# Performance work log

Measured on AMD Instinct MI355X. Metric: run time of the kernel, lower is better.

Reference implementation:

```python
import jax, jax.numpy as jnp
import numpy as np

WH, WW = 8, 8
DIM, HEADS = 512, 16
HEAD_DIM = DIM // HEADS
SCALE = HEAD_DIM ** (-0.5)
N = WH * WW
NW = 64  # number of windows sharing one mask


def _relative_position_index(wh, ww):
    ch, cw = np.meshgrid(np.arange(wh), np.arange(ww), indexing='ij')
    coords = np.stack([ch, cw]).reshape(2, -1)              # (2, N)
    rel = coords[:, :, None] - coords[:, None, :]           # (2, N, N)
    rel = rel.transpose(1, 2, 0).astype(np.int64)           # (N, N, 2)
    rel[:, :, 0] += wh - 1
    rel[:, :, 1] += ww - 1
    rel[:, :, 0] *= 2 * ww - 1
    return jnp.asarray(rel.sum(-1))                         # (N, N) int

_REL_IDX = _relative_position_index(WH, WW)


def setup_inputs() -> dict:
    key = jax.random.key(0)
    ks = jax.random.split(key, 10)
    B_ = 4096
    q = jax.random.normal(ks[0], (B_, N, DIM), dtype=jnp.float32)
    kv = jax.random.normal(ks[1], (B_, N, DIM), dtype=jnp.float32)
    mask = jax.random.normal(ks[2], (NW, N, N), dtype=jnp.float32)
    Wq = jax.random.normal(ks[3], (DIM, DIM), dtype=jnp.float32) * (DIM ** -0.5)
    bq = jnp.zeros((DIM,), dtype=jnp.float32)
    Wkv = jax.random.normal(ks[4], (DIM, 2 * DIM), dtype=jnp.float32) * (DIM ** -0.5)
    bkv = jnp.zeros((2 * DIM,), dtype=jnp.float32)
    bias_table = jax.random.normal(ks[5], ((2 * WH - 1) * (2 * WW - 1), HEADS), dtype=jnp.float32) * 0.02
    Wp = jax.random.normal(ks[6], (DIM, DIM), dtype=jnp.float32) * (DIM ** -0.5)
    bp = jnp.zeros((DIM,), dtype=jnp.float32)
    return {'q': q, 'kv': kv, 'mask': mask, 'Wq': Wq, 'bq': bq,
            'Wkv': Wkv, 'bkv': bkv, 'bias_table': bias_table, 'Wp': Wp, 'bp': bp}


def reference(q, kv, mask, Wq, bq, Wkv, bkv, bias_table, Wp, bp):
    B_, N_q, C = q.shape
    N_kv = kv.shape[1]
    # projections
    qh = (q @ Wq + bq).reshape(B_, N_q, HEADS, HEAD_DIM).transpose(0, 2, 1, 3)  # bhqd
    kvh = (kv @ Wkv + bkv).reshape(B_, N_kv, 2, HEADS, HEAD_DIM)
    k = kvh[:, :, 0].transpose(0, 2, 1, 3)   # bhkd
    v = kvh[:, :, 1].transpose(0, 2, 1, 3)   # bhkd
    attn = jnp.einsum('bhqd,bhkd->bhqk', qh * SCALE, k)
    # relative position bias: (N, N, H) -> (H, N, N)
    rpb = bias_table[_REL_IDX].transpose(2, 0, 1)
    attn = attn + rpb[None]
    # additive window mask
    nW = mask.shape[0]
    attn = attn.reshape(B_ // nW, nW, HEADS, N_q, N_kv) + mask[None, :, None]
    attn = attn.reshape(B_, HEADS, N_q, N_kv)
    attn = jax.nn.softmax(attn, axis=-1)
    x = jnp.einsum('bhqk,bhkd->bhqd', attn, v).transpose(0, 2, 1, 3).reshape(B_, N_q, C)
    return x @ Wp + bp
```

## Files before the change

### kernel.cpp

```cpp
#include <hip/hip_runtime.h>

typedef short bf16x8 __attribute__((ext_vector_type(8)));
typedef unsigned short u16x8 __attribute__((ext_vector_type(8)));
typedef float f32x4 __attribute__((ext_vector_type(4)));

#define MFMA16(a, b, c) __builtin_amdgcn_mfma_f32_16x16x32_bf16((a), (b), (c), 0, 0, 0)

#define SCALEF 0.17677669529663687f

__device__ __forceinline__ unsigned short f2bf(float f) {
  union { float f; unsigned u; } v; v.f = f;
  unsigned r = v.u + 0x7fffu + ((v.u >> 16) & 1u);
  return (unsigned short)(r >> 16);
}

__device__ __forceinline__ void gl_lds16(const void* g, void* l) {
  __builtin_amdgcn_global_load_lds(
      (const __attribute__((address_space(1))) void*)g,
      (__attribute__((address_space(3))) void*)l, 16, 0, 0);
}

__global__ __launch_bounds__(256) void transpose_cvt_k(const float* __restrict__ W,
    unsigned short* __restrict__ Wt, int K, int N) {
  int i = blockIdx.x * 256 + threadIdx.x;
  if (i >= N * K) return;
  int n = i / K, k = i - n * K;
  Wt[i] = f2bf(W[(long)k * N + n]);
}

__global__ __launch_bounds__(256) void build_rpb_k(const float* __restrict__ bt,
    float* __restrict__ rpb) {
  int i = blockIdx.x * 256 + threadIdx.x;
  if (i >= 16 * 64 * 64) return;
  int h = i >> 12, q = (i >> 6) & 63, k = i & 63;
  int dh = (q >> 3) - (k >> 3) + 7;
  int dw = (q & 7) - (k & 7) + 7;
  rpb[i] = bt[(dh * 15 + dw) * 16 + h];
}

__global__ __launch_bounds__(256) void cvt_bf16_k(const float* __restrict__ in,
    unsigned short* __restrict__ out, int n8) {
  int i = blockIdx.x * 256 + threadIdx.x;
  if (i >= n8) return;
  const float4* p = (const float4*)(in + (size_t)i * 8);
  float4 a = p[0], b = p[1];
  uint4 pk;
  pk.x = (unsigned)f2bf(a.x) | ((unsigned)f2bf(a.y) << 16);
  pk.y = (unsigned)f2bf(a.z) | ((unsigned)f2bf(a.w) << 16);
  pk.z = (unsigned)f2bf(b.x) | ((unsigned)f2bf(b.y) << 16);
  pk.w = (unsigned)f2bf(b.z) | ((unsigned)f2bf(b.w) << 16);
  *(uint4*)(out + (size_t)i * 8) = pk;
}

template <typename OT>
__device__ __forceinline__ void gemm_body(const unsigned short* __restrict__ A,
    const unsigned short* __restrict__ Bt, const float* __restrict__ bias,
    OT* __restrict__ C, int M, int N, int K)
{
  constexpr bool O_F32 = (sizeof(OT) == 4);

  __shared__ __align__(16) char smem[32768];
  unsigned short* Asm = (unsigned short*)smem;
  unsigned short* Bsm = Asm + 8192;

  const int tn = N >> 7;
  const int nbm = M >> 7;
  const int g = blockIdx.x;
  const int xcd = g & 7;
  const int s = g >> 3;
  const int bm = xcd * (nbm >> 3) + (s / tn);
  const int bn = s - (s / tn) * tn;

  const int tid = threadIdx.x;
  const int wave = tid >> 6, lane = tid & 63;
  const int wr = wave >> 1, wc = wave & 1;
  const int lg = lane >> 4, lc = lane & 15;

  const long rowBase = (long)bm * 128;
  const int colBase = bn * 128;
  const int KT = K >> 6;

  f32x4 acc[4][4];
#pragma unroll
  for (int i = 0; i < 4; ++i)
#pragma unroll
    for (int j = 0; j < 4; ++j)
      acc[i][j] = f32x4{0.f, 0.f, 0.f, 0.f};

  const int blr = lane >> 3;
  const int bsw = (lane & 7) ^ blr;

  auto issueA = [&](int kt) {
#pragma unroll
    for (int j = 0; j < 4; ++j) {
      int r = j * 32 + wave * 8 + blr;
      gl_lds16(A + (rowBase + r) * (long)K + kt * 64 + bsw * 8,
               Asm + (j * 4 + wave) * 512);
    }
  };
  auto issueB = [&](int kt) {
#pragma unroll
    for (int j = 0; j < 4; ++j) {
      int r = j * 32 + wave * 8 + blr;
      gl_lds16(Bt + (long)(colBase + r) * K + kt * 64 + bsw * 8,
               Bsm + (j * 4 + wave) * 512);
    }
  };
  auto compute = [&]() {
#pragma unroll
    for (int ks = 0; ks < 2; ++ks) {
      const int ca = (ks * 4 + lg) ^ (lc & 7);
      bf16x8 af[4], bfr[4];
#pragma unroll
      for (int mt = 0; mt < 4; ++mt)
        af[mt] = *(const bf16x8*)(Asm + (wr * 64 + mt * 16 + lc) * 64 + ca * 8);
#pragma unroll
      for (int nt = 0; nt < 4; ++nt)
        bfr[nt] = *(const bf16x8*)(Bsm + (wc * 64 + nt * 16 + lc) * 64 + ca * 8);
#pragma unroll
      for (int mt = 0; mt < 4; ++mt)
#pragma unroll
        for (int nt = 0; nt < 4; ++nt)
          acc[mt][nt] = MFMA16(af[mt], bfr[nt], acc[mt][nt]);
    }
  };

  issueA(0); issueB(0);
  __syncthreads();

  for (int kt = 0; kt < KT; ++kt) {
    const bool more = (kt + 1 < KT);
    compute();
    __syncthreads();
    if (more) {
      issueA(kt + 1); issueB(kt + 1);
      __syncthreads();
    }
  }

  float bv[4];
#pragma unroll
  for (int nt = 0; nt < 4; ++nt)
    bv[nt] = bias[colBase + wc * 64 + nt * 16 + lc];

  if constexpr (O_F32) {
    float* Sf = (float*)smem;
#pragma unroll
    for (int h = 0; h < 2; ++h) {
      if (wr == h) {
#pragma unroll
        for (int mt = 0; mt < 4; ++mt)
#pragma unroll
          for (int nt = 0; nt < 4; ++nt)
#pragma unroll
            for (int r = 0; r < 4; ++r)
              Sf[(mt * 16 + lg * 4 + r) * 128 + wc * 64 + nt * 16 + lc] =
                  acc[mt][nt][r] + bv[nt];
      }
      __syncthreads();
#pragma unroll
      for (int p = 0; p < 8; ++p) {
        int ch = p * 256 + tid, row = ch >> 5, c = ch & 31;
        *(float4*)((float*)C + (rowBase + h * 64 + row) * N + colBase + c * 4) =
            *(const float4*)(Sf + row * 128 + c * 4);
      }
      __syncthreads();
    }
  } else {
    unsigned short* Su = (unsigned short*)smem;
#pragma unroll
    for (int h = 0; h < 2; ++h) {
      if (wr == h) {
#pragma unroll
        for (int mt = 0; mt < 4; ++mt)
#pragma unroll
          for (int nt = 0; nt < 4; ++nt)
#pragma unroll
            for (int r = 0; r < 4; ++r)
              Su[(mt * 16 + lg * 4 + r) * 128 + wc * 64 + nt * 16 + lc] =
                  f2bf(acc[mt][nt][r] + bv[nt]);
      }
      __syncthreads();
#pragma unroll
      for (int p = 0; p < 4; ++p) {
        int ch = p * 256 + tid, row = ch >> 4, c = ch & 15;
        *(uint4*)((unsigned short*)C + (rowBase + h * 64 + row) * N + colBase + c * 8) =
            *(const uint4*)(Su + row * 128 + c * 8);
      }
      __syncthreads();
    }
  }
}

__global__ __launch_bounds__(256, 4) void gemm_q_k(const unsigned short* __restrict__ A,
    const unsigned short* __restrict__ Bt, const float* __restrict__ bias,
    unsigned short* __restrict__ C, int M, int N, int K) {
  gemm_body<unsigned short>(A, Bt, bias, C, M, N, K);
}
__global__ __launch_bounds__(256, 4) void gemm_kv_k(const unsigned short* __restrict__ A,
    const unsigned short* __restrict__ Bt, const float* __restrict__ bias,
    unsigned short* __restrict__ C, int M, int N, int K) {
  gemm_body<unsigned short>(A, Bt, bias, C, M, N, K);
}
__global__ __launch_bounds__(256, 4) void gemm_out_k(const unsigned short* __restrict__ A,
    const unsigned short* __restrict__ Bt, const float* __restrict__ bias,
    float* __restrict__ C, int M, int N, int K) {
  gemm_body<float>(A, Bt, bias, C, M, N, K);
}

__global__ __launch_bounds__(256) void attn_k(
    const unsigned short* __restrict__ qh,
    const unsigned short* __restrict__ kvh,
    const float* __restrict__ mask,
    const float* __restrict__ rpb,
    unsigned short* __restrict__ x)
{
  __shared__ unsigned short P[4][64][72];
  __shared__ unsigned short Vt[4][32][72];

  const int b = blockIdx.x;
  const int w = b & 63;
  const int tid = threadIdx.x;
  const int wave = tid >> 6, lane = tid & 63;
  const int lg = lane >> 4, lc = lane & 15;
  const long rowQ = (long)b * 64;

  for (int hi = 0; hi < 4; ++hi) {
    const int h = wave * 4 + hi;

    bf16x8 qf[4], kf[4];
#pragma unroll
    for (int mt = 0; mt < 4; ++mt)
      qf[mt] = *(const bf16x8*)(qh + (rowQ + mt * 16 + lc) * 512 + h * 32 + lg * 8);
#pragma unroll
    for (int nt = 0; nt < 4; ++nt)
      kf[nt] = *(const bf16x8*)(kvh + (rowQ + nt * 16 + lc) * 1024 + h * 32 + lg * 8);

    f32x4 acc[4][4];
#pragma unroll
    for (int mt = 0; mt < 4; ++mt)
#pragma unroll
      for (int nt = 0; nt < 4; ++nt)
        acc[mt][nt] = f32x4{0.f, 0.f, 0.f, 0.f};
#pragma unroll
    for (int mt = 0; mt < 4; ++mt)
#pragma unroll
      for (int nt = 0; nt < 4; ++nt)
        acc[mt][nt] = MFMA16(qf[mt], kf[nt], acc[mt][nt]);

    {
      const unsigned short* vp = kvh + (rowQ + lane) * 1024 + 512 + h * 32;
      u16x8 v0 = *(const u16x8*)(vp);
      u16x8 v1 = *(const u16x8*)(vp + 8);
      u16x8 v2 = *(const u16x8*)(vp + 16);
      u16x8 v3 = *(const u16x8*)(vp + 24);
#pragma unroll
      for (int j = 0; j < 8; ++j) {
        Vt[wave][j][lane]      = v0[j];
        Vt[wave][8 + j][lane]  = v1[j];
        Vt[wave][16 + j][lane] = v2[j];
        Vt[wave][24 + j][lane] = v3[j];
      }
    }

    float pden[4][4];
#pragma unroll
    for (int mt = 0; mt < 4; ++mt) {
#pragma unroll
      for (int r = 0; r < 4; ++r) {
        const int qrow = mt * 16 + lg * 4 + r;
        const float* rp = rpb + h * 4096 + qrow * 64 + lc;
        const float* mp = mask + w * 4096 + qrow * 64 + lc;
        float sc[4];
#pragma unroll
        for (int nt = 0; nt < 4; ++nt)
          sc[nt] = acc[mt][nt][r] * SCALEF + rp[nt * 16] + mp[nt * 16];
        float mx = fmaxf(fmaxf(sc[0], sc[1]), fmaxf(sc[2], sc[3]));
        mx = fmaxf(mx, __shfl_xor(mx, 1));
        mx = fmaxf(mx, __shfl_xor(mx, 2));
        mx = fmaxf(mx, __shfl_xor(mx, 4));
        mx = fmaxf(mx, __shfl_xor(mx, 8));
        float s = 0.f;
#pragma unroll
        for (int nt = 0; nt < 4; ++nt) { sc[nt] = __expf(sc[nt] - mx); s += sc[nt]; }
        s += __shfl_xor(s, 1);
        s += __shfl_xor(s, 2);
        s += __shfl_xor(s, 4);
        s += __shfl_xor(s, 8);
        pden[mt][r] = 1.f / s;
#pragma unroll
        for (int nt = 0; nt < 4; ++nt)
          P[wave][qrow][nt * 16 + lc] = f2bf(sc[nt]);
      }
    }

    f32x4 xacc[4][2];
#pragma unroll
    for (int mt = 0; mt < 4; ++mt)
#pragma unroll
      for (int nt = 0; nt < 2; ++nt)
        xacc[mt][nt] = f32x4{0.f, 0.f, 0.f, 0.f};
#pragma unroll
    for (int ks = 0; ks < 2; ++ks) {
      bf16x8 pa[4], vb[2];
#pragma unroll
      for (int mt = 0; mt < 4; ++mt)
        pa[mt] = *(const bf16x8*)&P[wave][mt * 16 + lc][ks * 32 + lg * 8];
#pragma unroll
      for (int nt = 0; nt < 2; ++nt)
        vb[nt] = *(const bf16x8*)&Vt[wave][nt * 16 + lc][ks * 32 + lg * 8];
#pragma unroll
      for (int mt = 0; mt < 4; ++mt)
#pragma unroll
        for (int nt = 0; nt < 2; ++nt)
          xacc[mt][nt] = MFMA16(pa[mt], vb[nt], xacc[mt][nt]);
    }

#pragma unroll
    for (int mt = 0; mt < 4; ++mt)
#pragma unroll
      for (int nt = 0; nt < 2; ++nt)
#pragma unroll
        for (int r = 0; r < 4; ++r) {
          const int qrow = mt * 16 + lg * 4 + r;
          x[(rowQ + qrow) * 512 + h * 32 + nt * 16 + lc] =
              f2bf(xacc[mt][nt][r] * pden[mt][r]);
        }
  }
}

extern "C" void kernel_launch(void* const* d_in, const int* in_sizes, int n_in,
                              void* d_out, int out_size, void* d_ws, size_t ws_size,
                              hipStream_t stream) {
  const float* q    = (const float*)d_in[0];
  const float* kv   = (const float*)d_in[1];
  const float* mask = (const float*)d_in[2];
  const float* Wq   = (const float*)d_in[3];
  const float* bq   = (const float*)d_in[4];
  const float* Wkv  = (const float*)d_in[5];
  const float* bkv  = (const float*)d_in[6];
  const float* btab = (const float*)d_in[7];
  const float* Wp   = (const float*)d_in[8];
  const float* bp   = (const float*)d_in[9];
  float* out = (float*)d_out;

  const int M = 4096 * 64;

  char* ws = (char*)d_ws;
  const size_t OFF_QH   = 0;
  const size_t OFF_KVH  = OFF_QH + (size_t)M * 512 * 2;
  const size_t OFF_SCR  = OFF_KVH + (size_t)M * 1024 * 2;
  const size_t OFF_WQT  = OFF_SCR + (size_t)M * 512 * 2;
  const size_t OFF_WKVT = OFF_WQT + 512 * 512 * 2;
  const size_t OFF_WPT  = OFF_WKVT + 1024 * 512 * 2;
  const size_t OFF_RPB  = OFF_WPT + 512 * 512 * 2;

  unsigned short* qh    = (unsigned short*)(ws + OFF_QH);
  unsigned short* kvh   = (unsigned short*)(ws + OFF_KVH);
  unsigned short* scr   = (unsigned short*)(ws + OFF_SCR);
  unsigned short* Wq_t  = (unsigned short*)(ws + OFF_WQT);
  unsigned short* Wkv_t = (unsigned short*)(ws + OFF_WKVT);
  unsigned short* Wp_t  = (unsigned short*)(ws + OFF_WPT);
  float* rpbf           = (float*)(ws + OFF_RPB);

  transpose_cvt_k<<<(512 * 512 + 255) / 256, 256, 0, stream>>>(Wq, Wq_t, 512, 512);
  transpose_cvt_k<<<(512 * 1024 + 255) / 256, 256, 0, stream>>>(Wkv, Wkv_t, 512, 1024);
  transpose_cvt_k<<<(512 * 512 + 255) / 256, 256, 0, stream>>>(Wp, Wp_t, 512, 512);
  build_rpb_k<<<(16 * 64 * 64 + 255) / 256, 256, 0, stream>>>(btab, rpbf);

  const int n8 = M * 512 / 8;

  cvt_bf16_k<<<n8 / 256, 256, 0, stream>>>(kv, scr, n8);
  gemm_kv_k<<<(M / 128) * (1024 / 128), 256, 0, stream>>>(scr, Wkv_t, bkv, kvh, M, 1024, 512);

  cvt_bf16_k<<<n8 / 256, 256, 0, stream>>>(q, scr, n8);
  gemm_q_k<<<(M / 128) * (512 / 128), 256, 0, stream>>>(scr, Wq_t, bq, qh, M, 512, 512);

  attn_k<<<4096, 256, 0, stream>>>(qh, kvh, mask, rpbf, scr);

  gemm_out_k<<<(M / 128) * (512 / 128), 256, 0, stream>>>(scr, Wp_t, bp, out, M, 512, 512);

  (void)in_sizes; (void)n_in; (void)out_size; (void)ws_size;
}
```

Measured before the change: 1.577 ms.

## Precombine bias+mask into swizzled table and prefetch next-head Q/K in attention

```diff
diff --git a/kernel.cpp b/kernel.cpp
--- a/kernel.cpp
+++ b/kernel.cpp
@@ -28,14 +28,15 @@
   Wt[i] = f2bf(W[(long)k * N + n]);
 }
 
-__global__ __launch_bounds__(256) void build_rpb_k(const float* __restrict__ bt,
-    float* __restrict__ rpb) {
+__global__ __launch_bounds__(256) void build_cb2_k(const float* __restrict__ bt,
+    const float* __restrict__ mask, float* __restrict__ cb2) {
   int i = blockIdx.x * 256 + threadIdx.x;
-  if (i >= 16 * 64 * 64) return;
-  int h = i >> 12, q = (i >> 6) & 63, k = i & 63;
+  if (i >= 64 * 16 * 64 * 64) return;
+  int nt = i & 3, lc = (i >> 2) & 15, q = (i >> 6) & 63, h = (i >> 12) & 15, w = i >> 16;
+  int k = nt * 16 + lc;
   int dh = (q >> 3) - (k >> 3) + 7;
   int dw = (q & 7) - (k & 7) + 7;
-  rpb[i] = bt[(dh * 15 + dw) * 16 + h];
+  cb2[i] = bt[(dh * 15 + dw) * 16 + h] + mask[w * 4096 + q * 64 + k];
 }
 
 __global__ __launch_bounds__(256) void cvt_bf16_k(const float* __restrict__ in,
@@ -208,15 +209,15 @@
   gemm_body<float>(A, Bt, bias, C, M, N, K);
 }
 
-__global__ __launch_bounds__(256) void attn_k(
+__global__ __launch_bounds__(256, 3) void attn_k(
     const unsigned short* __restrict__ qh,
     const unsigned short* __restrict__ kvh,
-    const float* __restrict__ mask,
-    const float* __restrict__ rpb,
+    const float* __restrict__ cb2,
     unsigned short* __restrict__ x)
 {
-  __shared__ unsigned short P[4][64][72];
-  __shared__ unsigned short Vt[4][32][72];
+  constexpr int LP = 68;
+  __shared__ unsigned short P[4][64][LP];
+  __shared__ unsigned short Vt[4][32][LP];
 
   const int b = blockIdx.x;
   const int w = b & 63;
@@ -225,16 +226,32 @@
   const int lg = lane >> 4, lc = lane & 15;
   const long rowQ = (long)b * 64;
 
+  bf16x8 qf[2][4], kf[2][4];
+  u16x8 vr[4];
+
+  auto loadQK = [&](int h, int s2) {
+#pragma unroll
+    for (int mt = 0; mt < 4; ++mt)
+      qf[s2][mt] = *(const bf16x8*)(qh + (rowQ + mt * 16 + lc) * 512 + h * 32 + lg * 8);
+#pragma unroll
+    for (int nt = 0; nt < 4; ++nt)
+      kf[s2][nt] = *(const bf16x8*)(kvh + (rowQ + nt * 16 + lc) * 1024 + h * 32 + lg * 8);
+  };
+
+  loadQK(wave * 4, 0);
+
+#pragma unroll
   for (int hi = 0; hi < 4; ++hi) {
+    const int cur = hi & 1;
     const int h = wave * 4 + hi;
 
-    bf16x8 qf[4], kf[4];
-#pragma unroll
-    for (int mt = 0; mt < 4; ++mt)
-      qf[mt] = *(const bf16x8*)(qh + (rowQ + mt * 16 + lc) * 512 + h * 32 + lg * 8);
-#pragma unroll
-    for (int nt = 0; nt < 4; ++nt)
-      kf[nt] = *(const bf16x8*)(kvh + (rowQ + nt * 16 + lc) * 1024 + h * 32 + lg * 8);
+    {
+      const unsigned short* vp = kvh + (rowQ + lane) * 1024 + 512 + h * 32;
+      vr[0] = *(const u16x8*)(vp);
+      vr[1] = *(const u16x8*)(vp + 8);
+      vr[2] = *(const u16x8*)(vp + 16);
+      vr[3] = *(const u16x8*)(vp + 24);
+    }
 
     f32x4 acc[4][4];
 #pragma unroll
@@ -246,35 +263,22 @@
     for (int mt = 0; mt < 4; ++mt)
 #pragma unroll
       for (int nt = 0; nt < 4; ++nt)
-        acc[mt][nt] = MFMA16(qf[mt], kf[nt], acc[mt][nt]);
-
-    {
-      const unsigned short* vp = kvh + (rowQ + lane) * 1024 + 512 + h * 32;
-      u16x8 v0 = *(const u16x8*)(vp);
-      u16x8 v1 = *(const u16x8*)(vp + 8);
-      u16x8 v2 = *(const u16x8*)(vp + 16);
-      u16x8 v3 = *(const u16x8*)(vp + 24);
-#pragma unroll
-      for (int j = 0; j < 8; ++j) {
-        Vt[wave][j][lane]      = v0[j];
-        Vt[wave][8 + j][lane]  = v1[j];
-        Vt[wave][16 + j][lane] = v2[j];
-        Vt[wave][24 + j][lane] = v3[j];
-      }
-    }
-
+        acc[mt][nt] = MFMA16(qf[cur][mt], kf[cur][nt], acc[mt][nt]);
+
+    if (hi < 3) loadQK(h + 1, cur ^ 1);
+
+    const float* cbq = cb2 + (((size_t)(w * 16 + h)) << 12) + lc * 4;
     float pden[4][4];
 #pragma unroll
     for (int mt = 0; mt < 4; ++mt) {
 #pragma unroll
       for (int r = 0; r < 4; ++r) {
         const int qrow = mt * 16 + lg * 4 + r;
-        const float* rp = rpb + h * 4096 + qrow * 64 + lc;
-        const float* mp = mask + w * 4096 + qrow * 64 + lc;
+        f32x4 cb = *(const f32x4*)(cbq + qrow * 64);
         float sc[4];
 #pragma unroll
         for (int nt = 0; nt < 4; ++nt)
-          sc[nt] = acc[mt][nt][r] * SCALEF + rp[nt * 16] + mp[nt * 16];
+          sc[nt] = acc[mt][nt][r] * SCALEF + cb[nt];
         float mx = fmaxf(fmaxf(sc[0], sc[1]), fmaxf(sc[2], sc[3]));
         mx = fmaxf(mx, __shfl_xor(mx, 1));
         mx = fmaxf(mx, __shfl_xor(mx, 2));
@@ -292,6 +296,14 @@
         for (int nt = 0; nt < 4; ++nt)
           P[wave][qrow][nt * 16 + lc] = f2bf(sc[nt]);
       }
+    }
+
+#pragma unroll
+    for (int j = 0; j < 8; ++j) {
+      Vt[wave][j][lane]      = vr[0][j];
+      Vt[wave][8 + j][lane]  = vr[1][j];
+      Vt[wave][16 + j][lane] = vr[2][j];
+      Vt[wave][24 + j][lane] = vr[3][j];
     }
 
     f32x4 xacc[4][2];
@@ -353,7 +365,7 @@
   const size_t OFF_WQT  = OFF_SCR + (size_t)M * 512 * 2;
   const size_t OFF_WKVT = OFF_WQT + 512 * 512 * 2;
   const size_t OFF_WPT  = OFF_WKVT + 1024 * 512 * 2;
-  const size_t OFF_RPB  = OFF_WPT + 512 * 512 * 2;
+  const size_t OFF_CB2  = OFF_WPT + 512 * 512 * 2;
 
   unsigned short* qh    = (unsigned short*)(ws + OFF_QH);
   unsigned short* kvh   = (unsigned short*)(ws + OFF_KVH);
@@ -361,12 +373,12 @@
   unsigned short* Wq_t  = (unsigned short*)(ws + OFF_WQT);
   unsigned short* Wkv_t = (unsigned short*)(ws + OFF_WKVT);
   unsigned short* Wp_t  = (unsigned short*)(ws + OFF_WPT);
-  float* rpbf           = (float*)(ws + OFF_RPB);
+  float* cb2f           = (float*)(ws + OFF_CB2);
 
   transpose_cvt_k<<<(512 * 512 + 255) / 256, 256, 0, stream>>>(Wq, Wq_t, 512, 512);
   transpose_cvt_k<<<(512 * 1024 + 255) / 256, 256, 0, stream>>>(Wkv, Wkv_t, 512, 1024);
   transpose_cvt_k<<<(512 * 512 + 255) / 256, 256, 0, stream>>>(Wp, Wp_t, 512, 512);
-  build_rpb_k<<<(16 * 64 * 64 + 255) / 256, 256, 0, stream>>>(btab, rpbf);
+  build_cb2_k<<<(64 * 16 * 64 * 64) / 256, 256, 0, stream>>>(btab, mask, cb2f);
 
   const int n8 = M * 512 / 8;
 
@@ -376,7 +388,7 @@
   cvt_bf16_k<<<n8 / 256, 256, 0, stream>>>(q, scr, n8);
   gemm_q_k<<<(M / 128) * (512 / 128), 256, 0, stream>>>(scr, Wq_t, bq, qh, M, 512, 512);
 
-  attn_k<<<4096, 256, 0, stream>>>(qh, kvh, mask, rpbf, scr);
+  attn_k<<<4096, 256, 0, stream>>>(qh, kvh, cb2f, scr);
 
   gemm_out_k<<<(M / 128) * (512 / 128), 256, 0, stream>>>(scr, Wp_t, bp, out, M, 512, 512);
 
```

New measurement: 1.622 ms. 2.8% more time.

## Restructure attention kernel: per-wave query rows, shared V/mask in LDS, scale folded into Wq

Applied to the files above, without the earlier changes.

```diff
diff --git a/kernel.cpp b/kernel.cpp
--- a/kernel.cpp
+++ b/kernel.cpp
@@ -13,6 +13,10 @@
   unsigned r = v.u + 0x7fffu + ((v.u >> 16) & 1u);
   return (unsigned short)(r >> 16);
 }
+__device__ __forceinline__ float bf2f(unsigned short b) {
+  union { unsigned u; float f; } v; v.u = ((unsigned)b) << 16;
+  return v.f;
+}
 
 __device__ __forceinline__ void gl_lds16(const void* g, void* l) {
   __builtin_amdgcn_global_load_lds(
@@ -21,21 +25,28 @@
 }
 
 __global__ __launch_bounds__(256) void transpose_cvt_k(const float* __restrict__ W,
-    unsigned short* __restrict__ Wt, int K, int N) {
+    unsigned short* __restrict__ Wt, int K, int N, float scale) {
   int i = blockIdx.x * 256 + threadIdx.x;
   if (i >= N * K) return;
   int n = i / K, k = i - n * K;
-  Wt[i] = f2bf(W[(long)k * N + n]);
-}
-
-__global__ __launch_bounds__(256) void build_rpb_k(const float* __restrict__ bt,
-    float* __restrict__ rpb) {
+  Wt[i] = f2bf(W[(long)k * N + n] * scale);
+}
+
+__global__ __launch_bounds__(256) void scale_bias_k(const float* __restrict__ b,
+    float* __restrict__ bs, float scale, int n) {
+  int i = blockIdx.x * 256 + threadIdx.x;
+  if (i < n) bs[i] = b[i] * scale;
+}
+
+__global__ __launch_bounds__(256) void build_rpbp_k(const float* __restrict__ bt,
+    float* __restrict__ rpbp) {
   int i = blockIdx.x * 256 + threadIdx.x;
   if (i >= 16 * 64 * 64) return;
-  int h = i >> 12, q = (i >> 6) & 63, k = i & 63;
+  int kt = i & 3, lcv = (i >> 2) & 15, q = (i >> 6) & 63, h = i >> 12;
+  int k = kt * 16 + lcv;
   int dh = (q >> 3) - (k >> 3) + 7;
   int dw = (q & 7) - (k & 7) + 7;
-  rpb[i] = bt[(dh * 15 + dw) * 16 + h];
+  rpbp[i] = bt[(dh * 15 + dw) * 16 + h];
 }
 
 __global__ __launch_bounds__(256) void cvt_bf16_k(const float* __restrict__ in,
@@ -208,15 +219,17 @@
   gemm_body<float>(A, Bt, bias, C, M, N, K);
 }
 
-__global__ __launch_bounds__(256) void attn_k(
+__global__ __launch_bounds__(256, 5) void attn_k(
     const unsigned short* __restrict__ qh,
     const unsigned short* __restrict__ kvh,
     const float* __restrict__ mask,
-    const float* __restrict__ rpb,
+    const float* __restrict__ rpbp,
     unsigned short* __restrict__ x)
 {
-  __shared__ unsigned short P[4][64][72];
-  __shared__ unsigned short Vt[4][32][72];
+  __shared__ unsigned short P[64][68];
+  __shared__ unsigned short Vt[2][32][68];
+  __shared__ unsigned short maskS[64][68];
+  __shared__ unsigned short xs[4][16][40];
 
   const int b = blockIdx.x;
   const int w = b & 63;
@@ -225,107 +238,99 @@
   const int lg = lane >> 4, lc = lane & 15;
   const long rowQ = (long)b * 64;
 
-  for (int hi = 0; hi < 4; ++hi) {
-    const int h = wave * 4 + hi;
-
-    bf16x8 qf[4], kf[4];
-#pragma unroll
-    for (int mt = 0; mt < 4; ++mt)
-      qf[mt] = *(const bf16x8*)(qh + (rowQ + mt * 16 + lc) * 512 + h * 32 + lg * 8);
-#pragma unroll
-    for (int nt = 0; nt < 4; ++nt)
-      kf[nt] = *(const bf16x8*)(kvh + (rowQ + nt * 16 + lc) * 1024 + h * 32 + lg * 8);
-
-    f32x4 acc[4][4];
-#pragma unroll
-    for (int mt = 0; mt < 4; ++mt)
-#pragma unroll
-      for (int nt = 0; nt < 4; ++nt)
-        acc[mt][nt] = f32x4{0.f, 0.f, 0.f, 0.f};
-#pragma unroll
-    for (int mt = 0; mt < 4; ++mt)
-#pragma unroll
-      for (int nt = 0; nt < 4; ++nt)
-        acc[mt][nt] = MFMA16(qf[mt], kf[nt], acc[mt][nt]);
-
+#pragma unroll
+  for (int t = 0; t < 16; ++t) {
+    int i = t * 256 + tid;
+    int qq = i >> 6, k = i & 63;
+    maskS[qq][(k & 15) * 4 + (k >> 4)] = f2bf(mask[w * 4096 + i]);
+  }
+
+  const int vtok = tid >> 2, vg = tid & 3;
+  const unsigned short* vbase = kvh + (rowQ + vtok) * 1024 + 512 + vg * 8;
+
+  {
+    u16x8 v0 = *(const u16x8*)(vbase);
+#pragma unroll
+    for (int j = 0; j < 8; ++j) Vt[0][vg * 8 + j][vtok] = v0[j];
+  }
+  __syncthreads();
+
+  for (int h = 0; h < 16; ++h) {
+    const int cur = h & 1;
+
+    u16x8 vn;
+    if (h < 15) vn = *(const u16x8*)(vbase + (h + 1) * 32);
+
+    bf16x8 qf = *(const bf16x8*)(qh + (rowQ + wave * 16 + lc) * 512 + h * 32 + lg * 8);
+    bf16x8 kf[4];
+#pragma unroll
+    for (int kt = 0; kt < 4; ++kt)
+      kf[kt] = *(const bf16x8*)(kvh + (rowQ + kt * 16 + lc) * 1024 + h * 32 + lg * 8);
+
+    f32x4 acc[4];
+#pragma unroll
+    for (int kt = 0; kt < 4; ++kt) acc[kt] = f32x4{0.f, 0.f, 0.f, 0.f};
+#pragma unroll
+    for (int kt = 0; kt < 4; ++kt) acc[kt] = MFMA16(qf, kf[kt], acc[kt]);
+
+    float pden[4];
+#pragma unroll
+    for (int r = 0; r < 4; ++r) {
+      const int qrow = wave * 16 + lg * 4 + r;
+      f32x4 rp = *(const f32x4*)(rpbp + (h << 12) + qrow * 64 + lc * 4);
+      ushort4 mv = *(const ushort4*)&maskS[qrow][lc * 4];
+      float sc[4];
+      sc[0] = acc[0][r] + rp[0] + bf2f(mv.x);
+      sc[1] = acc[1][r] + rp[1] + bf2f(mv.y);
+      sc[2] = acc[2][r] + rp[2] + bf2f(mv.z);
+      sc[3] = acc[3][r] + rp[3] + bf2f(mv.w);
+      float mx = fmaxf(fmaxf(sc[0], sc[1]), fmaxf(sc[2], sc[3]));
+      mx = fmaxf(mx, __shfl_xor(mx, 1));
+      mx = fmaxf(mx, __shfl_xor(mx, 2));
+      mx = fmaxf(mx, __shfl_xor(mx, 4));
+      mx = fmaxf(mx, __shfl_xor(mx, 8));
+      float s = 0.f;
+#pragma unroll
+      for (int kt = 0; kt < 4; ++kt) { sc[kt] = __expf(sc[kt] - mx); s += sc[kt]; }
+      s += __shfl_xor(s, 1);
+      s += __shfl_xor(s, 2);
+      s += __shfl_xor(s, 4);
+      s += __shfl_xor(s, 8);
+      pden[r] = 1.f / s;
+#pragma unroll
+      for (int kt = 0; kt < 4; ++kt)
+        P[qrow][kt * 16 + lc] = f2bf(sc[kt]);
+    }
+
+    if (h < 15) {
+#pragma unroll
+      for (int j = 0; j < 8; ++j) Vt[cur ^ 1][vg * 8 + j][vtok] = vn[j];
+    }
+
+    f32x4 xacc[2];
+    xacc[0] = f32x4{0.f, 0.f, 0.f, 0.f};
+    xacc[1] = f32x4{0.f, 0.f, 0.f, 0.f};
+#pragma unroll
+    for (int ks = 0; ks < 2; ++ks) {
+      bf16x8 pa = *(const bf16x8*)&P[wave * 16 + lc][ks * 32 + lg * 8];
+      bf16x8 vb0 = *(const bf16x8*)&Vt[cur][lc][ks * 32 + lg * 8];
+      bf16x8 vb1 = *(const bf16x8*)&Vt[cur][16 + lc][ks * 32 + lg * 8];
+      xacc[0] = MFMA16(pa, vb0, xacc[0]);
+      xacc[1] = MFMA16(pa, vb1, xacc[1]);
+    }
+
+#pragma unroll
+    for (int dt = 0; dt < 2; ++dt)
+#pragma unroll
+      for (int r = 0; r < 4; ++r)
+        xs[wave][lg * 4 + r][dt * 16 + lc] = f2bf(xacc[dt][r] * pden[r]);
     {
-      const unsigned short* vp = kvh + (rowQ + lane) * 1024 + 512 + h * 32;
-      u16x8 v0 = *(const u16x8*)(vp);
-      u16x8 v1 = *(const u16x8*)(vp + 8);
-      u16x8 v2 = *(const u16x8*)(vp + 16);
-      u16x8 v3 = *(const u16x8*)(vp + 24);
-#pragma unroll
-      for (int j = 0; j < 8; ++j) {
-        Vt[wave][j][lane]      = v0[j];
-        Vt[wave][8 + j][lane]  = v1[j];
-        Vt[wave][16 + j][lane] = v2[j];
-        Vt[wave][24 + j][lane] = v3[j];
-      }
-    }
-
-    float pden[4][4];
-#pragma unroll
-    for (int mt = 0; mt < 4; ++mt) {
-#pragma unroll
-      for (int r = 0; r < 4; ++r) {
-        const int qrow = mt * 16 + lg * 4 + r;
-        const float* rp = rpb + h * 4096 + qrow * 64 + lc;
-        const float* mp = mask + w * 4096 + qrow * 64 + lc;
-        float sc[4];
-#pragma unroll
-        for (int nt = 0; nt < 4; ++nt)
-          sc[nt] = acc[mt][nt][r] * SCALEF + rp[nt * 16] + mp[nt * 16];
-        float mx = fmaxf(fmaxf(sc[0], sc[1]), fmaxf(sc[2], sc[3]));
-        mx = fmaxf(mx, __shfl_xor(mx, 1));
-        mx = fmaxf(mx, __shfl_xor(mx, 2));
-        mx = fmaxf(mx, __shfl_xor(mx, 4));
-        mx = fmaxf(mx, __shfl_xor(mx, 8));
-        float s = 0.f;
-#pragma unroll
-        for (int nt = 0; nt < 4; ++nt) { sc[nt] = __expf(sc[nt] - mx); s += sc[nt]; }
-        s += __shfl_xor(s, 1);
-        s += __shfl_xor(s, 2);
-        s += __shfl_xor(s, 4);
-        s += __shfl_xor(s, 8);
-        pden[mt][r] = 1.f / s;
-#pragma unroll
-        for (int nt = 0; nt < 4; ++nt)
-          P[wave][qrow][nt * 16 + lc] = f2bf(sc[nt]);
-      }
-    }
-
-    f32x4 xacc[4][2];
-#pragma unroll
-    for (int mt = 0; mt < 4; ++mt)
-#pragma unroll
-      for (int nt = 0; nt < 2; ++nt)
-        xacc[mt][nt] = f32x4{0.f, 0.f, 0.f, 0.f};
-#pragma unroll
-    for (int ks = 0; ks < 2; ++ks) {
-      bf16x8 pa[4], vb[2];
-#pragma unroll
-      for (int mt = 0; mt < 4; ++mt)
-        pa[mt] = *(const bf16x8*)&P[wave][mt * 16 + lc][ks * 32 + lg * 8];
-#pragma unroll
-      for (int nt = 0; nt < 2; ++nt)
-        vb[nt] = *(const bf16x8*)&Vt[wave][nt * 16 + lc][ks * 32 + lg * 8];
-#pragma unroll
-      for (int mt = 0; mt < 4; ++mt)
-#pragma unroll
-        for (int nt = 0; nt < 2; ++nt)
-          xacc[mt][nt] = MFMA16(pa[mt], vb[nt], xacc[mt][nt]);
-    }
-
-#pragma unroll
-    for (int mt = 0; mt < 4; ++mt)
-#pragma unroll
-      for (int nt = 0; nt < 2; ++nt)
-#pragma unroll
-        for (int r = 0; r < 4; ++r) {
-          const int qrow = mt * 16 + lg * 4 + r;
-          x[(rowQ + qrow) * 512 + h * 32 + nt * 16 + lc] =
-              f2bf(xacc[mt][nt][r] * pden[mt][r]);
-        }
+      int row = lane >> 2, c = lane & 3;
+      uint4 v = *(const uint4*)&xs[wave][row][c * 8];
+      *(uint4*)(x + (rowQ + wave * 16 + row) * 512 + h * 32 + c * 8) = v;
+    }
+
+    __syncthreads();
   }
 }
 
@@ -353,7 +358,8 @@
   const size_t OFF_WQT  = OFF_SCR + (size_t)M * 512 * 2;
   const size_t OFF_WKVT = OFF_WQT + 512 * 512 * 2;
   const size_t OFF_WPT  = OFF_WKVT + 1024 * 512 * 2;
-  const size_t OFF_RPB  = OFF_WPT + 512 * 512 * 2;
+  const size_t OFF_RPBP = OFF_WPT + 512 * 512 * 2;
+  const size_t OFF_BQS  = OFF_RPBP + 16 * 64 * 64 * 4;
 
   unsigned short* qh    = (unsigned short*)(ws + OFF_QH);
   unsigned short* kvh   = (unsigned short*)(ws + OFF_KVH);
@@ -361,12 +367,14 @@
   unsigned short* Wq_t  = (unsigned short*)(ws + OFF_WQT);
   unsigned short* Wkv_t = (unsigned short*)(ws + OFF_WKVT);
   unsigned short* Wp_t  = (unsigned short*)(ws + OFF_WPT);
-  float* rpbf           = (float*)(ws + OFF_RPB);
-
-  transpose_cvt_k<<<(512 * 512 + 255) / 256, 256, 0, stream>>>(Wq, Wq_t, 512, 512);
-  transpose_cvt_k<<<(512 * 1024 + 255) / 256, 256, 0, stream>>>(Wkv, Wkv_t, 512, 1024);
-  transpose_cvt_k<<<(512 * 512 + 255) / 256, 256, 0, stream>>>(Wp, Wp_t, 512, 512);
-  build_rpb_k<<<(16 * 64 * 64 + 255) / 256, 256, 0, stream>>>(btab, rpbf);
+  float* rpbp           = (float*)(ws + OFF_RPBP);
+  float* bq_s           = (float*)(ws + OFF_BQS);
+
+  transpose_cvt_k<<<(512 * 512 + 255) / 256, 256, 0, stream>>>(Wq, Wq_t, 512, 512, SCALEF);
+  transpose_cvt_k<<<(512 * 1024 + 255) / 256, 256, 0, stream>>>(Wkv, Wkv_t, 512, 1024, 1.0f);
+  transpose_cvt_k<<<(512 * 512 + 255) / 256, 256, 0, stream>>>(Wp, Wp_t, 512, 512, 1.0f);
+  scale_bias_k<<<2, 256, 0, stream>>>(bq, bq_s, SCALEF, 512);
+  build_rpbp_k<<<(16 * 64 * 64) / 256, 256, 0, stream>>>(btab, rpbp);
 
   const int n8 = M * 512 / 8;
 
@@ -374,9 +382,9 @@
   gemm_kv_k<<<(M / 128) * (1024 / 128), 256, 0, stream>>>(scr, Wkv_t, bkv, kvh, M, 1024, 512);
 
   cvt_bf16_k<<<n8 / 256, 256, 0, stream>>>(q, scr, n8);
-  gemm_q_k<<<(M / 128) * (512 / 128), 256, 0, stream>>>(scr, Wq_t, bq, qh, M, 512, 512);
-
-  attn_k<<<4096, 256, 0, stream>>>(qh, kvh, mask, rpbf, scr);
+  gemm_q_k<<<(M / 128) * (512 / 128), 256, 0, stream>>>(scr, Wq_t, bq_s, qh, M, 512, 512);
+
+  attn_k<<<4096, 256, 0, stream>>>(qh, kvh, mask, rpbp, scr);
 
   gemm_out_k<<<(M / 128) * (512 / 128), 256, 0, stream>>>(scr, Wp_t, bp, out, M, 512, 512);
 
```

Result: faster. 1.381 ms (-12.4%).
